# Performance work log

Hardware: AMD Instinct MI355X
Metric: run time of the kernel (lower is better)

## Reference

```python
import jax, jax.numpy as jnp
import numpy as np

EPS = 1e-06


def _phi(x):
    # elu_feature_map: elu(x) + 1  (strictly positive features)
    return jax.nn.elu(x) + 1.0


def setup_inputs() -> dict:
    key = jax.random.key(0)
    k1, k2, k3 = jax.random.split(key, 3)
    N, L, H, D = 4, 4096, 12, 64
    q = jax.random.normal(k1, (N, L, H, D), dtype=jnp.float32)
    k = jax.random.normal(k2, (N, L, H, D), dtype=jnp.float32)
    v = jax.random.normal(k3, (N, L, H, D), dtype=jnp.float32)
    return {"q": q, "k": k, "v": v}


def _causal_linear_attention(q, k, v):
    qf = _phi(q)  # [N,L,H,D]
    kf = _phi(k)
    # normalizer: z_l = q_l . (sum_{s<=l} k_s) + eps
    z = jnp.einsum('nlhd,nlhd->nlh', qf, jnp.cumsum(kf, axis=1)) + EPS
    # causal_dot_product: sequential cumulative outer-product scan over L
    q_l = jnp.moveaxis(qf, 1, 0)  # [L,N,H,D]
    k_l = jnp.moveaxis(kf, 1, 0)
    v_l = jnp.moveaxis(v, 1, 0)   # [L,N,H,M]
    N, H, D = qf.shape[0], qf.shape[2], qf.shape[3]
    M = v.shape[3]
    S0 = jnp.zeros((N, H, D, M), dtype=qf.dtype)

    def step(S, qkv):
        ql, kl, vl = qkv
        S = S + jnp.einsum('nhd,nhm->nhdm', kl, vl)  # accumulate k v^T
        o = jnp.einsum('nhd,nhdm->nhm', ql, S)       # q . S
        return S, o

    _, out = jax.lax.scan(step, S0, (q_l, k_l, v_l))  # out: [L,N,H,M]
    out = jnp.moveaxis(out, 0, 1)  # [N,L,H,M]
    return out / z[..., None]


def reference(q, k, v):
    # mask=None path of LinearAttention.forward (causal linear attention)
    return _causal_linear_attention(q, k, v)
```

## Files before the change

kernel.cpp:

```cpp
#include <hip/hip_runtime.h>


#define NBATCH 4
#define LSEQ   4096
#define NHEAD  12
#define DDIM   64
#define LSTRIDE (NHEAD * DDIM)
#define NH     (NBATCH * NHEAD)
#define EPSF   1e-6f
#define CHUNK  64
#define NUMC   (LSEQ / CHUNK)
#define SB     72

typedef __attribute__((ext_vector_type(8))) short bf16x8;
typedef __attribute__((ext_vector_type(4))) float f32x4;

__device__ __forceinline__ float phi(float x) { return x > 0.f ? x + 1.f : __expf(x); }

__device__ __forceinline__ unsigned short f2bf(float x) {
    union { float f; unsigned u; } v; v.f = x;
    unsigned r = v.u + 0x7fffu + ((v.u >> 16) & 1u);
    return (unsigned short)(r >> 16);
}
__device__ __forceinline__ float bf2f(short s) {
    union { float f; unsigned u; } v; v.u = ((unsigned)(unsigned short)s) << 16;
    return v.f;
}
__device__ __forceinline__ uint2 pack4(float4 a) {
    uint2 r;
    r.x = (unsigned)f2bf(a.x) | ((unsigned)f2bf(a.y) << 16);
    r.y = (unsigned)f2bf(a.z) | ((unsigned)f2bf(a.w) << 16);
    return r;
}

__device__ __forceinline__ float4 xpose4(float4 x, int lane) {
    const bool b0 = (lane >> 4) & 1, b1 = (lane >> 5) & 1;
    float s0 = b0 ? x.x : x.y;
    float s1 = b0 ? x.z : x.w;
    s0 = __shfl_xor(s0, 16);
    s1 = __shfl_xor(s1, 16);
    float4 y;
    if (b0) { y.x = s0;  y.y = x.y; y.z = s1;  y.w = x.w; }
    else    { y.x = x.x; y.y = s0;  y.z = x.z; y.w = s1;  }
    float t0 = b1 ? y.x : y.z;
    float t1 = b1 ? y.y : y.w;
    t0 = __shfl_xor(t0, 32);
    t1 = __shfl_xor(t1, 32);
    float4 z;
    if (b1) { z.x = t0;  z.y = t1;  z.z = y.z; z.w = y.w; }
    else    { z.x = y.x; z.y = y.y; z.z = t0;  z.w = t1;  }
    return z;
}

__global__ __launch_bounds__(256) void k_sum_mf(const float* __restrict__ kin,
                                                const float* __restrict__ vin,
                                                float* __restrict__ kvws,
                                                float* __restrict__ ksws) {
    __shared__ short sKT[64 * SB];
    __shared__ short sVT[64 * SB];
    const int b = blockIdx.x, seq = b / NUMC, c = b % NUMC;
    const int n0 = seq / NHEAD, h0 = seq % NHEAD;
    const int t = threadIdx.x;
    const int gbase = ((n0 * LSEQ + c * CHUNK) * NHEAD + h0) * DDIM;
    const int lane = t & 63, w = t >> 6;
    const int nn = lane & 15, qq = lane >> 4;

#pragma unroll
    for (int rep = 0; rep < 4; ++rep) {
        const int row = rep * 16 + 4 * w + qq;
        const int c4 = nn << 2;
        const int l0 = rep * 16 + 4 * w;
        float4 kk = *(const float4*)(kin + gbase + row * LSTRIDE + c4);
        float4 kp = {phi(kk.x), phi(kk.y), phi(kk.z), phi(kk.w)};
        float4 kt = xpose4(kp, lane);
        *(uint2*)(sKT + (c4 + qq) * SB + l0) = pack4(kt);
        float4 vv = *(const float4*)(vin + gbase + row * LSTRIDE + c4);
        float4 vt = xpose4(vv, lane);
        *(uint2*)(sVT + (c4 + qq) * SB + l0) = pack4(vt);
    }
    __syncthreads();

    const int rowM = 16 * w + nn;
    bf16x8 af0 = *(const bf16x8*)(sVT + rowM * SB + qq * 8);
    bf16x8 af1 = *(const bf16x8*)(sVT + rowM * SB + 32 + qq * 8);
    float* kvb = kvws + (size_t)b * DDIM * DDIM;
    float ks = 0.f;

#pragma unroll
    for (int ct = 0; ct < 4; ++ct) {
        bf16x8 bf0 = *(const bf16x8*)(sKT + (16 * ct + nn) * SB + qq * 8);
        bf16x8 bf1 = *(const bf16x8*)(sKT + (16 * ct + nn) * SB + 32 + qq * 8);
        f32x4 acc = {0.f, 0.f, 0.f, 0.f};
        acc = __builtin_amdgcn_mfma_f32_16x16x32_bf16(af0, bf0, acc, 0, 0, 0);
        acc = __builtin_amdgcn_mfma_f32_16x16x32_bf16(af1, bf1, acc, 0, 0, 0);
        if (ct == w) {
            float s = 0.f;
#pragma unroll
            for (int j = 0; j < 8; ++j) s += bf2f(bf0[j]) + bf2f(bf1[j]);
            s += __shfl_xor(s, 16);
            s += __shfl_xor(s, 32);
            ks = s;
        }
#pragma unroll
        for (int r = 0; r < 4; ++r)
            kvb[(16 * w + 4 * qq + r) * DDIM + 16 * ct + nn] = acc[r];
    }
    if (qq == 0) ksws[b * DDIM + 16 * w + nn] = ks;
}

__global__ __launch_bounds__(64) void k_scan_mm(float* __restrict__ kv,
                                                float* __restrict__ ksum) {
    const int bid = blockIdx.x;
    const int seq = bid >> 4, part = bid & 15;
    const int t = threadIdx.x;
    float4* base = (float4*)(kv + (size_t)seq * NUMC * DDIM * DDIM) + part * 64 + t;
    float4 S = {0.f, 0.f, 0.f, 0.f};
#pragma unroll 4
    for (int c = 0; c < NUMC; ++c) {
        float4 x = base[c * (DDIM * DDIM / 4)];
        base[c * (DDIM * DDIM / 4)] = S;
        S.x += x.x; S.y += x.y; S.z += x.z; S.w += x.w;
    }
    if (part == 0) {
        float s = 0.0f;
        float* kb = ksum + (size_t)seq * NUMC * DDIM + t;
        for (int c = 0; c < NUMC; ++c) {
            float x = kb[c * DDIM];
            kb[c * DDIM] = s;
            s += x;
        }
    }
}

__global__ __launch_bounds__(256) void k_out_mf(const float* __restrict__ qin,
                                                const float* __restrict__ kin,
                                                const float* __restrict__ vin,
                                                const float* __restrict__ kvws,
                                                const float* __restrict__ ksws,
                                                float* __restrict__ out) {
    __shared__ short sQ [64 * SB];
    __shared__ short sKA[64 * SB];
    __shared__ short sVT[64 * SB];
    __shared__ short sST[64 * SB];
    __shared__ float sKs[64];
    __shared__ float sZq[64];

    const int b = blockIdx.x, seq = b / NUMC, c = b % NUMC;
    const int n0 = seq / NHEAD, h0 = seq % NHEAD;
    const int t = threadIdx.x;
    const int gbase = ((n0 * LSEQ + c * CHUNK) * NHEAD + h0) * DDIM;
    const int lane = t & 63, w = t >> 6;
    const int nn = lane & 15, qq = lane >> 4;

    if (t < 64) sKs[t] = ksws[b * DDIM + t];

    const float* Sg = kvws + (size_t)b * DDIM * DDIM;
#pragma unroll
    for (int rep = 0; rep < 4; ++rep) {
        const int row = rep * 16 + 4 * w + qq;
        const int c4 = nn << 2;
        const int l0 = rep * 16 + 4 * w;
        float4 qv = *(const float4*)(qin + gbase + row * LSTRIDE + c4);
        float4 kk = *(const float4*)(kin + gbase + row * LSTRIDE + c4);
        float4 qp = {phi(qv.x), phi(qv.y), phi(qv.z), phi(qv.w)};
        float4 kp = {phi(kk.x), phi(kk.y), phi(kk.z), phi(kk.w)};
        *(uint2*)(sQ  + row * SB + c4) = pack4(qp);
        *(uint2*)(sKA + row * SB + c4) = pack4(kp);
        float4 sv = *(const float4*)(Sg + row * 64 + c4);
        *(uint2*)(sST + row * SB + c4) = pack4(sv);
        float4 vv = *(const float4*)(vin + gbase + row * LSTRIDE + c4);
        float4 vt = xpose4(vv, lane);
        *(uint2*)(sVT + (c4 + qq) * SB + l0) = pack4(vt);
    }
    __syncthreads();

    const int rowA = 16 * w + nn;
    bf16x8 qf0 = *(const bf16x8*)(sQ + rowA * SB + qq * 8);
    bf16x8 qf1 = *(const bf16x8*)(sQ + rowA * SB + 32 + qq * 8);
    float am[4][4];
    float zrow[4] = {0.f, 0.f, 0.f, 0.f};
#pragma unroll
    for (int ct = 0; ct < 4; ++ct) {
        bf16x8 kf0 = *(const bf16x8*)(sKA + (16 * ct + nn) * SB + qq * 8);
        bf16x8 kf1 = *(const bf16x8*)(sKA + (16 * ct + nn) * SB + 32 + qq * 8);
        f32x4 acc = {0.f, 0.f, 0.f, 0.f};
        acc = __builtin_amdgcn_mfma_f32_16x16x32_bf16(qf0, kf0, acc, 0, 0, 0);
        acc = __builtin_amdgcn_mfma_f32_16x16x32_bf16(qf1, kf1, acc, 0, 0, 0);
#pragma unroll
        for (int r = 0; r < 4; ++r) {
            const int ri = 16 * w + 4 * qq + r, cj = 16 * ct + nn;
            const float mval = (cj <= ri) ? acc[r] : 0.f;
            am[ct][r] = mval;
            zrow[r] += mval;
        }
    }
#pragma unroll
    for (int r = 0; r < 4; ++r) {
        float s = zrow[r];
        s += __shfl_xor(s, 1); s += __shfl_xor(s, 2);
        s += __shfl_xor(s, 4); s += __shfl_xor(s, 8);
        zrow[r] = s;
    }
    float zq = 0.f;
#pragma unroll
    for (int j = 0; j < 8; ++j) {
        zq += bf2f(qf0[j]) * sKs[qq * 8 + j];
        zq += bf2f(qf1[j]) * sKs[32 + qq * 8 + j];
    }
    zq += __shfl_xor(zq, 16);
    zq += __shfl_xor(zq, 32);

    __syncthreads();
    if (qq == 0) sZq[16 * w + nn] = zq;
#pragma unroll
    for (int ct = 0; ct < 4; ++ct)
#pragma unroll
        for (int r = 0; r < 4; ++r)
            sKA[(16 * w + 4 * qq + r) * SB + 16 * ct + nn] = (short)f2bf(am[ct][r]);
    __syncthreads();

    f32x4 o[4] = {{0,0,0,0},{0,0,0,0},{0,0,0,0},{0,0,0,0}};
    bf16x8 af0 = *(const bf16x8*)(sKA + rowA * SB + qq * 8);
    bf16x8 af1 = *(const bf16x8*)(sKA + rowA * SB + 32 + qq * 8);
#pragma unroll
    for (int ct = 0; ct < 4; ++ct) {
        bf16x8 vf0 = *(const bf16x8*)(sVT + (16 * ct + nn) * SB + qq * 8);
        bf16x8 vf1 = *(const bf16x8*)(sVT + (16 * ct + nn) * SB + 32 + qq * 8);
        o[ct] = __builtin_amdgcn_mfma_f32_16x16x32_bf16(af0, vf0, o[ct], 0, 0, 0);
        o[ct] = __builtin_amdgcn_mfma_f32_16x16x32_bf16(af1, vf1, o[ct], 0, 0, 0);
        bf16x8 sf0 = *(const bf16x8*)(sST + (16 * ct + nn) * SB + qq * 8);
        bf16x8 sf1 = *(const bf16x8*)(sST + (16 * ct + nn) * SB + 32 + qq * 8);
        o[ct] = __builtin_amdgcn_mfma_f32_16x16x32_bf16(qf0, sf0, o[ct], 0, 0, 0);
        o[ct] = __builtin_amdgcn_mfma_f32_16x16x32_bf16(qf1, sf1, o[ct], 0, 0, 0);
    }

#pragma unroll
    for (int r = 0; r < 4; ++r) {
        const int ri = 16 * w + 4 * qq + r;
        const float z = zrow[r] + sZq[ri] + EPSF;
        const float invz = 1.f / z;
#pragma unroll
        for (int ct = 0; ct < 4; ++ct)
            out[gbase + ri * LSTRIDE + 16 * ct + nn] = o[ct][r] * invz;
    }
}

__global__ __launch_bounds__(64) void k_seq(const float* __restrict__ qin,
                                            const float* __restrict__ kin,
                                            const float* __restrict__ vin,
                                            float* __restrict__ out) {
    const int seq = blockIdx.x;
    const int n = seq / NHEAD, h = seq % NHEAD;
    const int lane = threadIdx.x;
    float Scol[DDIM];
#pragma unroll
    for (int d = 0; d < DDIM; ++d) Scol[d] = 0.0f;
    float kc = 0.0f;
    __shared__ float qk[2 * DDIM];
    int base = (n * LSEQ * NHEAD + h) * DDIM + lane;
    for (int i = 0; i < LSEQ; ++i) {
        float qval = phi(qin[base]);
        float kval = phi(kin[base]);
        float vval = vin[base];
        kc += kval;
        float zp = qval * kc;
#pragma unroll
        for (int off = 32; off > 0; off >>= 1) zp += __shfl_xor(zp, off, 64);
        float z = zp + EPSF;
        qk[2 * lane] = kval;
        qk[2 * lane + 1] = qval;
        __syncthreads();
        const float4* qk4 = (const float4*)qk;
        float acc = 0.0f;
#pragma unroll
        for (int d2 = 0; d2 < DDIM / 2; ++d2) {
            float4 t0 = qk4[d2];
            int d = 2 * d2;
            Scol[d]     += t0.x * vval;  acc += t0.y * Scol[d];
            Scol[d + 1] += t0.z * vval;  acc += t0.w * Scol[d + 1];
        }
        out[base] = acc / z;
        base += LSTRIDE;
        __syncthreads();
    }
}

extern "C" void kernel_launch(void* const* d_in, const int* in_sizes, int n_in,
                              void* d_out, int out_size, void* d_ws, size_t ws_size,
                              hipStream_t stream) {
    const float* q = (const float*)d_in[0];
    const float* k = (const float*)d_in[1];
    const float* v = (const float*)d_in[2];
    float* out = (float*)d_out;
    float* ws  = (float*)d_ws;

    const size_t need = (size_t)NH * NUMC * (DDIM * DDIM + DDIM) * sizeof(float);
    if (ws_size >= need) {
        float* kv   = ws;
        float* ksum = ws + (size_t)NH * NUMC * DDIM * DDIM;
        k_sum_mf<<<NH * NUMC, 256, 0, stream>>>(k, v, kv, ksum);
        k_scan_mm<<<NH * 16, 64, 0, stream>>>(kv, ksum);
        k_out_mf<<<NH * NUMC, 256, 0, stream>>>(q, k, v, kv, ksum, out);
    } else {
        k_seq<<<NH, 64, 0, stream>>>(q, k, v, out);
    }
}
```

Before: 223.3 us.

## Group chunks into partitions and carry running state through a fused per-partition loop

Each block now handles a partition of 4 consecutive chunks instead of one. The sum kernel accumulates the partition's k^T v state in registers, so only 16 partial states per sequence are written and scanned instead of 64. The output kernel keeps the running state in registers and updates it chunk by chunk with MFMAs, and prefetches the next chunk's inputs into registers. This cuts workspace traffic and the length of the scan. The cost is fewer blocks (768), more serial work per block, and an extra shared buffer that may reduce occupancy.

```diff
diff --git a/kernel.cpp b/kernel.cpp
--- a/kernel.cpp
+++ b/kernel.cpp
@@ -10,6 +10,8 @@
 #define EPSF   1e-6f
 #define CHUNK  64
 #define NUMC   (LSEQ / CHUNK)
+#define PPART  16
+#define CPP    (NUMC / PPART)
 #define SB     72
 
 typedef __attribute__((ext_vector_type(8))) short bf16x8;
@@ -52,196 +54,261 @@
     return z;
 }
 
-__global__ __launch_bounds__(256) void k_sum_mf(const float* __restrict__ kin,
-                                                const float* __restrict__ vin,
-                                                float* __restrict__ kvws,
-                                                float* __restrict__ ksws) {
+__global__ __launch_bounds__(256) void k_psum(const float* __restrict__ kin,
+                                              const float* __restrict__ vin,
+                                              float* __restrict__ kvws,
+                                              float* __restrict__ ksws) {
     __shared__ short sKT[64 * SB];
     __shared__ short sVT[64 * SB];
-    const int b = blockIdx.x, seq = b / NUMC, c = b % NUMC;
+    const int b = blockIdx.x, seq = b / PPART, p = b % PPART;
     const int n0 = seq / NHEAD, h0 = seq % NHEAD;
     const int t = threadIdx.x;
-    const int gbase = ((n0 * LSEQ + c * CHUNK) * NHEAD + h0) * DDIM;
     const int lane = t & 63, w = t >> 6;
     const int nn = lane & 15, qq = lane >> 4;
-
-#pragma unroll
-    for (int rep = 0; rep < 4; ++rep) {
-        const int row = rep * 16 + 4 * w + qq;
-        const int c4 = nn << 2;
-        const int l0 = rep * 16 + 4 * w;
-        float4 kk = *(const float4*)(kin + gbase + row * LSTRIDE + c4);
-        float4 kp = {phi(kk.x), phi(kk.y), phi(kk.z), phi(kk.w)};
-        float4 kt = xpose4(kp, lane);
-        *(uint2*)(sKT + (c4 + qq) * SB + l0) = pack4(kt);
-        float4 vv = *(const float4*)(vin + gbase + row * LSTRIDE + c4);
-        float4 vt = xpose4(vv, lane);
-        *(uint2*)(sVT + (c4 + qq) * SB + l0) = pack4(vt);
-    }
-    __syncthreads();
-
-    const int rowM = 16 * w + nn;
-    bf16x8 af0 = *(const bf16x8*)(sVT + rowM * SB + qq * 8);
-    bf16x8 af1 = *(const bf16x8*)(sVT + rowM * SB + 32 + qq * 8);
-    float* kvb = kvws + (size_t)b * DDIM * DDIM;
+    const int c4 = nn << 2;
+
+    float4 kreg[4], vreg[4];
+    auto LOADCC = [&](int cc) {
+        const int gb = ((n0 * LSEQ + (p * CPP + cc) * CHUNK) * NHEAD + h0) * DDIM;
+#pragma unroll
+        for (int rep = 0; rep < 4; ++rep) {
+            const int r16 = rep * 16 + 4 * w + qq;
+            kreg[rep] = *(const float4*)(kin + gb + r16 * LSTRIDE + c4);
+            vreg[rep] = *(const float4*)(vin + gb + r16 * LSTRIDE + c4);
+        }
+    };
+
+    f32x4 S[4] = {{0,0,0,0},{0,0,0,0},{0,0,0,0},{0,0,0,0}};
     float ks = 0.f;
-
-#pragma unroll
-    for (int ct = 0; ct < 4; ++ct) {
-        bf16x8 bf0 = *(const bf16x8*)(sKT + (16 * ct + nn) * SB + qq * 8);
-        bf16x8 bf1 = *(const bf16x8*)(sKT + (16 * ct + nn) * SB + 32 + qq * 8);
-        f32x4 acc = {0.f, 0.f, 0.f, 0.f};
-        acc = __builtin_amdgcn_mfma_f32_16x16x32_bf16(af0, bf0, acc, 0, 0, 0);
-        acc = __builtin_amdgcn_mfma_f32_16x16x32_bf16(af1, bf1, acc, 0, 0, 0);
-        if (ct == w) {
-            float s = 0.f;
-#pragma unroll
-            for (int j = 0; j < 8; ++j) s += bf2f(bf0[j]) + bf2f(bf1[j]);
-            s += __shfl_xor(s, 16);
-            s += __shfl_xor(s, 32);
-            ks = s;
-        }
+    LOADCC(0);
+    for (int cc = 0; cc < CPP; ++cc) {
+#pragma unroll
+        for (int rep = 0; rep < 4; ++rep) {
+            const int l0 = rep * 16 + 4 * w;
+            float4 kk = kreg[rep];
+            float4 kp = {phi(kk.x), phi(kk.y), phi(kk.z), phi(kk.w)};
+            float4 kt = xpose4(kp, lane);
+            *(uint2*)(sKT + (c4 + qq) * SB + l0) = pack4(kt);
+            float4 vt = xpose4(vreg[rep], lane);
+            *(uint2*)(sVT + (c4 + qq) * SB + l0) = pack4(vt);
+        }
+        __syncthreads();
+        if (cc + 1 < CPP) LOADCC(cc + 1);
+        const int rowM = 16 * w + nn;
+        bf16x8 af0 = *(const bf16x8*)(sVT + rowM * SB + qq * 8);
+        bf16x8 af1 = *(const bf16x8*)(sVT + rowM * SB + 32 + qq * 8);
+#pragma unroll
+        for (int ct = 0; ct < 4; ++ct) {
+            bf16x8 bf0 = *(const bf16x8*)(sKT + (16 * ct + nn) * SB + qq * 8);
+            bf16x8 bf1 = *(const bf16x8*)(sKT + (16 * ct + nn) * SB + 32 + qq * 8);
+            S[ct] = __builtin_amdgcn_mfma_f32_16x16x32_bf16(af0, bf0, S[ct], 0, 0, 0);
+            S[ct] = __builtin_amdgcn_mfma_f32_16x16x32_bf16(af1, bf1, S[ct], 0, 0, 0);
+            if (ct == w) {
+                float s = 0.f;
+#pragma unroll
+                for (int j = 0; j < 8; ++j) s += bf2f(bf0[j]) + bf2f(bf1[j]);
+                s += __shfl_xor(s, 16);
+                s += __shfl_xor(s, 32);
+                ks += s;
+            }
+        }
+        __syncthreads();
+    }
+    float* kvb = kvws + (size_t)b * (DDIM * DDIM);
+#pragma unroll
+    for (int ct = 0; ct < 4; ++ct)
 #pragma unroll
         for (int r = 0; r < 4; ++r)
-            kvb[(16 * w + 4 * qq + r) * DDIM + 16 * ct + nn] = acc[r];
-    }
+            kvb[(16 * w + 4 * qq + r) * DDIM + 16 * ct + nn] = S[ct][r];
     if (qq == 0) ksws[b * DDIM + 16 * w + nn] = ks;
 }
 
-__global__ __launch_bounds__(64) void k_scan_mm(float* __restrict__ kv,
-                                                float* __restrict__ ksum) {
+__global__ __launch_bounds__(64) void k_scanP(float* __restrict__ kv,
+                                              float* __restrict__ ksum) {
     const int bid = blockIdx.x;
     const int seq = bid >> 4, part = bid & 15;
     const int t = threadIdx.x;
-    float4* base = (float4*)(kv + (size_t)seq * NUMC * DDIM * DDIM) + part * 64 + t;
+    float4* base = (float4*)(kv + (size_t)seq * PPART * DDIM * DDIM) + part * 64 + t;
+    float4 x[PPART];
+#pragma unroll
+    for (int c = 0; c < PPART; ++c) x[c] = base[c * (DDIM * DDIM / 4)];
     float4 S = {0.f, 0.f, 0.f, 0.f};
-#pragma unroll 4
-    for (int c = 0; c < NUMC; ++c) {
-        float4 x = base[c * (DDIM * DDIM / 4)];
+#pragma unroll
+    for (int c = 0; c < PPART; ++c) {
         base[c * (DDIM * DDIM / 4)] = S;
-        S.x += x.x; S.y += x.y; S.z += x.z; S.w += x.w;
+        S.x += x[c].x; S.y += x[c].y; S.z += x[c].z; S.w += x[c].w;
     }
     if (part == 0) {
-        float s = 0.0f;
-        float* kb = ksum + (size_t)seq * NUMC * DDIM + t;
-        for (int c = 0; c < NUMC; ++c) {
-            float x = kb[c * DDIM];
-            kb[c * DDIM] = s;
-            s += x;
-        }
-    }
-}
-
-__global__ __launch_bounds__(256) void k_out_mf(const float* __restrict__ qin,
-                                                const float* __restrict__ kin,
-                                                const float* __restrict__ vin,
-                                                const float* __restrict__ kvws,
-                                                const float* __restrict__ ksws,
-                                                float* __restrict__ out) {
+        float* kb = ksum + (size_t)seq * PPART * DDIM + t;
+        float xs[PPART];
+#pragma unroll
+        for (int c = 0; c < PPART; ++c) xs[c] = kb[c * DDIM];
+        float s = 0.f;
+#pragma unroll
+        for (int c = 0; c < PPART; ++c) { kb[c * DDIM] = s; s += xs[c]; }
+    }
+}
+
+__global__ __launch_bounds__(256, 3) void k_fused(const float* __restrict__ qin,
+                                                  const float* __restrict__ kin,
+                                                  const float* __restrict__ vin,
+                                                  const float* __restrict__ kvws,
+                                                  const float* __restrict__ ksws,
+                                                  float* __restrict__ out) {
     __shared__ short sQ [64 * SB];
     __shared__ short sKA[64 * SB];
+    __shared__ short sKT[64 * SB];
     __shared__ short sVT[64 * SB];
     __shared__ short sST[64 * SB];
     __shared__ float sKs[64];
     __shared__ float sZq[64];
 
-    const int b = blockIdx.x, seq = b / NUMC, c = b % NUMC;
+    const int b = blockIdx.x, seq = b / PPART, p = b % PPART;
     const int n0 = seq / NHEAD, h0 = seq % NHEAD;
     const int t = threadIdx.x;
-    const int gbase = ((n0 * LSEQ + c * CHUNK) * NHEAD + h0) * DDIM;
     const int lane = t & 63, w = t >> 6;
     const int nn = lane & 15, qq = lane >> 4;
+    const int c4 = nn << 2;
 
     if (t < 64) sKs[t] = ksws[b * DDIM + t];
 
-    const float* Sg = kvws + (size_t)b * DDIM * DDIM;
-#pragma unroll
-    for (int rep = 0; rep < 4; ++rep) {
-        const int row = rep * 16 + 4 * w + qq;
-        const int c4 = nn << 2;
-        const int l0 = rep * 16 + 4 * w;
-        float4 qv = *(const float4*)(qin + gbase + row * LSTRIDE + c4);
-        float4 kk = *(const float4*)(kin + gbase + row * LSTRIDE + c4);
-        float4 qp = {phi(qv.x), phi(qv.y), phi(qv.z), phi(qv.w)};
-        float4 kp = {phi(kk.x), phi(kk.y), phi(kk.z), phi(kk.w)};
-        *(uint2*)(sQ  + row * SB + c4) = pack4(qp);
-        *(uint2*)(sKA + row * SB + c4) = pack4(kp);
-        float4 sv = *(const float4*)(Sg + row * 64 + c4);
-        *(uint2*)(sST + row * SB + c4) = pack4(sv);
-        float4 vv = *(const float4*)(vin + gbase + row * LSTRIDE + c4);
-        float4 vt = xpose4(vv, lane);
-        *(uint2*)(sVT + (c4 + qq) * SB + l0) = pack4(vt);
-    }
-    __syncthreads();
-
-    const int rowA = 16 * w + nn;
-    bf16x8 qf0 = *(const bf16x8*)(sQ + rowA * SB + qq * 8);
-    bf16x8 qf1 = *(const bf16x8*)(sQ + rowA * SB + 32 + qq * 8);
-    float am[4][4];
-    float zrow[4] = {0.f, 0.f, 0.f, 0.f};
+    const float* Sg = kvws + (size_t)b * (DDIM * DDIM);
+    f32x4 Sreg[4];
 #pragma unroll
     for (int ct = 0; ct < 4; ++ct) {
-        bf16x8 kf0 = *(const bf16x8*)(sKA + (16 * ct + nn) * SB + qq * 8);
-        bf16x8 kf1 = *(const bf16x8*)(sKA + (16 * ct + nn) * SB + 32 + qq * 8);
-        f32x4 acc = {0.f, 0.f, 0.f, 0.f};
-        acc = __builtin_amdgcn_mfma_f32_16x16x32_bf16(qf0, kf0, acc, 0, 0, 0);
-        acc = __builtin_amdgcn_mfma_f32_16x16x32_bf16(qf1, kf1, acc, 0, 0, 0);
 #pragma unroll
         for (int r = 0; r < 4; ++r) {
-            const int ri = 16 * w + 4 * qq + r, cj = 16 * ct + nn;
-            const float mval = (cj <= ri) ? acc[r] : 0.f;
-            am[ct][r] = mval;
-            zrow[r] += mval;
-        }
-    }
-#pragma unroll
-    for (int r = 0; r < 4; ++r) {
-        float s = zrow[r];
-        s += __shfl_xor(s, 1); s += __shfl_xor(s, 2);
-        s += __shfl_xor(s, 4); s += __shfl_xor(s, 8);
-        zrow[r] = s;
-    }
-    float zq = 0.f;
-#pragma unroll
-    for (int j = 0; j < 8; ++j) {
-        zq += bf2f(qf0[j]) * sKs[qq * 8 + j];
-        zq += bf2f(qf1[j]) * sKs[32 + qq * 8 + j];
-    }
-    zq += __shfl_xor(zq, 16);
-    zq += __shfl_xor(zq, 32);
-
-    __syncthreads();
-    if (qq == 0) sZq[16 * w + nn] = zq;
-#pragma unroll
-    for (int ct = 0; ct < 4; ++ct)
-#pragma unroll
-        for (int r = 0; r < 4; ++r)
-            sKA[(16 * w + 4 * qq + r) * SB + 16 * ct + nn] = (short)f2bf(am[ct][r]);
-    __syncthreads();
-
-    f32x4 o[4] = {{0,0,0,0},{0,0,0,0},{0,0,0,0},{0,0,0,0}};
-    bf16x8 af0 = *(const bf16x8*)(sKA + rowA * SB + qq * 8);
-    bf16x8 af1 = *(const bf16x8*)(sKA + rowA * SB + 32 + qq * 8);
-#pragma unroll
-    for (int ct = 0; ct < 4; ++ct) {
-        bf16x8 vf0 = *(const bf16x8*)(sVT + (16 * ct + nn) * SB + qq * 8);
-        bf16x8 vf1 = *(const bf16x8*)(sVT + (16 * ct + nn) * SB + 32 + qq * 8);
-        o[ct] = __builtin_amdgcn_mfma_f32_16x16x32_bf16(af0, vf0, o[ct], 0, 0, 0);
-        o[ct] = __builtin_amdgcn_mfma_f32_16x16x32_bf16(af1, vf1, o[ct], 0, 0, 0);
-        bf16x8 sf0 = *(const bf16x8*)(sST + (16 * ct + nn) * SB + qq * 8);
-        bf16x8 sf1 = *(const bf16x8*)(sST + (16 * ct + nn) * SB + 32 + qq * 8);
-        o[ct] = __builtin_amdgcn_mfma_f32_16x16x32_bf16(qf0, sf0, o[ct], 0, 0, 0);
-        o[ct] = __builtin_amdgcn_mfma_f32_16x16x32_bf16(qf1, sf1, o[ct], 0, 0, 0);
-    }
-
-#pragma unroll
-    for (int r = 0; r < 4; ++r) {
-        const int ri = 16 * w + 4 * qq + r;
-        const float z = zrow[r] + sZq[ri] + EPSF;
-        const float invz = 1.f / z;
+            const float sv = Sg[(16 * w + 4 * qq + r) * DDIM + 16 * ct + nn];
+            Sreg[ct][r] = sv;
+            sST[(16 * w + 4 * qq + r) * SB + 16 * ct + nn] = (short)f2bf(sv);
+        }
+    }
+
+    float4 qreg[4], kreg[4], vreg[4];
+    auto LOADCC = [&](int cc) {
+        const int gb = ((n0 * LSEQ + (p * CPP + cc) * CHUNK) * NHEAD + h0) * DDIM;
+#pragma unroll
+        for (int rep = 0; rep < 4; ++rep) {
+            const int r16 = rep * 16 + 4 * w + qq;
+            qreg[rep] = *(const float4*)(qin + gb + r16 * LSTRIDE + c4);
+            kreg[rep] = *(const float4*)(kin + gb + r16 * LSTRIDE + c4);
+            vreg[rep] = *(const float4*)(vin + gb + r16 * LSTRIDE + c4);
+        }
+    };
+    LOADCC(0);
+
+    for (int cc = 0; cc < CPP; ++cc) {
+        const int gbase = ((n0 * LSEQ + (p * CPP + cc) * CHUNK) * NHEAD + h0) * DDIM;
+#pragma unroll
+        for (int rep = 0; rep < 4; ++rep) {
+            const int row = rep * 16 + 4 * w + qq;
+            const int l0 = rep * 16 + 4 * w;
+            float4 qv = qreg[rep];
+            float4 qp = {phi(qv.x), phi(qv.y), phi(qv.z), phi(qv.w)};
+            *(uint2*)(sQ + row * SB + c4) = pack4(qp);
+            float4 kk = kreg[rep];
+            float4 kp = {phi(kk.x), phi(kk.y), phi(kk.z), phi(kk.w)};
+            *(uint2*)(sKA + row * SB + c4) = pack4(kp);
+            float4 kt = xpose4(kp, lane);
+            *(uint2*)(sKT + (c4 + qq) * SB + l0) = pack4(kt);
+            float4 vt = xpose4(vreg[rep], lane);
+            *(uint2*)(sVT + (c4 + qq) * SB + l0) = pack4(vt);
+        }
+        __syncthreads();
+
+        const int rowA = 16 * w + nn;
+        bf16x8 qf0 = *(const bf16x8*)(sQ + rowA * SB + qq * 8);
+        bf16x8 qf1 = *(const bf16x8*)(sQ + rowA * SB + 32 + qq * 8);
+        float am[4][4];
+        float zrow[4] = {0.f, 0.f, 0.f, 0.f};
+#pragma unroll
+        for (int ct = 0; ct < 4; ++ct) {
+            bf16x8 kf0 = *(const bf16x8*)(sKA + (16 * ct + nn) * SB + qq * 8);
+            bf16x8 kf1 = *(const bf16x8*)(sKA + (16 * ct + nn) * SB + 32 + qq * 8);
+            f32x4 acc = {0.f, 0.f, 0.f, 0.f};
+            acc = __builtin_amdgcn_mfma_f32_16x16x32_bf16(qf0, kf0, acc, 0, 0, 0);
+            acc = __builtin_amdgcn_mfma_f32_16x16x32_bf16(qf1, kf1, acc, 0, 0, 0);
+#pragma unroll
+            for (int r = 0; r < 4; ++r) {
+                const int ri = 16 * w + 4 * qq + r, cj = 16 * ct + nn;
+                const float mval = (cj <= ri) ? acc[r] : 0.f;
+                am[ct][r] = mval;
+                zrow[r] += mval;
+            }
+        }
+#pragma unroll
+        for (int r = 0; r < 4; ++r) {
+            float s = zrow[r];
+            s += __shfl_xor(s, 1); s += __shfl_xor(s, 2);
+            s += __shfl_xor(s, 4); s += __shfl_xor(s, 8);
+            zrow[r] = s;
+        }
+        float zq = 0.f;
+#pragma unroll
+        for (int j = 0; j < 8; ++j) {
+            zq += bf2f(qf0[j]) * sKs[qq * 8 + j];
+            zq += bf2f(qf1[j]) * sKs[32 + qq * 8 + j];
+        }
+        zq += __shfl_xor(zq, 16);
+        zq += __shfl_xor(zq, 32);
+
+        __syncthreads();
+        if (qq == 0) sZq[16 * w + nn] = zq;
 #pragma unroll
         for (int ct = 0; ct < 4; ++ct)
-            out[gbase + ri * LSTRIDE + 16 * ct + nn] = o[ct][r] * invz;
+#pragma unroll
+            for (int r = 0; r < 4; ++r)
+                sKA[(16 * w + 4 * qq + r) * SB + 16 * ct + nn] = (short)f2bf(am[ct][r]);
+        __syncthreads();
+
+        if (cc + 1 < CPP) LOADCC(cc + 1);
+
+        f32x4 o[4] = {{0,0,0,0},{0,0,0,0},{0,0,0,0},{0,0,0,0}};
+        bf16x8 af0 = *(const bf16x8*)(sKA + rowA * SB + qq * 8);
+        bf16x8 af1 = *(const bf16x8*)(sKA + rowA * SB + 32 + qq * 8);
+        bf16x8 av0 = *(const bf16x8*)(sVT + rowA * SB + qq * 8);
+        bf16x8 av1 = *(const bf16x8*)(sVT + rowA * SB + 32 + qq * 8);
+        float ksc = 0.f;
+#pragma unroll
+        for (int ct = 0; ct < 4; ++ct) {
+            bf16x8 vf0 = *(const bf16x8*)(sVT + (16 * ct + nn) * SB + qq * 8);
+            bf16x8 vf1 = *(const bf16x8*)(sVT + (16 * ct + nn) * SB + 32 + qq * 8);
+            o[ct] = __builtin_amdgcn_mfma_f32_16x16x32_bf16(af0, vf0, o[ct], 0, 0, 0);
+            o[ct] = __builtin_amdgcn_mfma_f32_16x16x32_bf16(af1, vf1, o[ct], 0, 0, 0);
+            bf16x8 sf0 = *(const bf16x8*)(sST + (16 * ct + nn) * SB + qq * 8);
+            bf16x8 sf1 = *(const bf16x8*)(sST + (16 * ct + nn) * SB + 32 + qq * 8);
+            o[ct] = __builtin_amdgcn_mfma_f32_16x16x32_bf16(qf0, sf0, o[ct], 0, 0, 0);
+            o[ct] = __builtin_amdgcn_mfma_f32_16x16x32_bf16(qf1, sf1, o[ct], 0, 0, 0);
+            bf16x8 kt0 = *(const bf16x8*)(sKT + (16 * ct + nn) * SB + qq * 8);
+            bf16x8 kt1 = *(const bf16x8*)(sKT + (16 * ct + nn) * SB + 32 + qq * 8);
+            Sreg[ct] = __builtin_amdgcn_mfma_f32_16x16x32_bf16(av0, kt0, Sreg[ct], 0, 0, 0);
+            Sreg[ct] = __builtin_amdgcn_mfma_f32_16x16x32_bf16(av1, kt1, Sreg[ct], 0, 0, 0);
+            if (ct == w) {
+                float s = 0.f;
+#pragma unroll
+                for (int j = 0; j < 8; ++j) s += bf2f(kt0[j]) + bf2f(kt1[j]);
+                s += __shfl_xor(s, 16);
+                s += __shfl_xor(s, 32);
+                ksc = s;
+            }
+        }
+
+#pragma unroll
+        for (int r = 0; r < 4; ++r) {
+            const int ri = 16 * w + 4 * qq + r;
+            const float z = zrow[r] + sZq[ri] + EPSF;
+            const float invz = 1.f / z;
+#pragma unroll
+            for (int ct = 0; ct < 4; ++ct)
+                out[gbase + ri * LSTRIDE + 16 * ct + nn] = o[ct][r] * invz;
+        }
+        __syncthreads();
+#pragma unroll
+        for (int ct = 0; ct < 4; ++ct)
+#pragma unroll
+            for (int r = 0; r < 4; ++r)
+                sST[(16 * w + 4 * qq + r) * SB + 16 * ct + nn] = (short)f2bf(Sreg[ct][r]);
+        if (qq == 0) sKs[16 * w + nn] += ksc;
     }
 }
 
@@ -294,13 +361,13 @@
     float* out = (float*)d_out;
     float* ws  = (float*)d_ws;
 
-    const size_t need = (size_t)NH * NUMC * (DDIM * DDIM + DDIM) * sizeof(float);
+    const size_t need = (size_t)NH * PPART * (DDIM * DDIM + DDIM) * sizeof(float);
     if (ws_size >= need) {
         float* kv   = ws;
-        float* ksum = ws + (size_t)NH * NUMC * DDIM * DDIM;
-        k_sum_mf<<<NH * NUMC, 256, 0, stream>>>(k, v, kv, ksum);
-        k_scan_mm<<<NH * 16, 64, 0, stream>>>(kv, ksum);
-        k_out_mf<<<NH * NUMC, 256, 0, stream>>>(q, k, v, kv, ksum, out);
+        float* ksum = ws + (size_t)NH * PPART * DDIM * DDIM;
+        k_psum <<<NH * PPART, 256, 0, stream>>>(k, v, kv, ksum);
+        k_scanP<<<NH * PPART,  64, 0, stream>>>(kv, ksum);
+        k_fused<<<NH * PPART, 256, 0, stream>>>(q, k, v, kv, ksum, out);
     } else {
         k_seq<<<NH, 64, 0, stream>>>(q, k, v, out);
     }
```

Result: faster. 206.9 us (-7.4%).
